# Optimization experiments

Hardware: AMD Instinct MI355X
Metric: run time of the kernel (lower is better)

## Reference

```python
import jax, jax.numpy as jnp
import numpy as np

B, L_IN, L_OUT, N, COV, EMB, H = 32, 336, 48, 512, 4, 32, 64
C = 1 + COV
D_IN = EMB + COV


def setup_inputs() -> dict:
    key = jax.random.key(0)
    ks = jax.random.split(key, 16)
    s = 1.0 / np.sqrt(H)

    def rn(k, shape, scale):
        return jax.random.normal(k, shape, jnp.float32) * scale

    return {
        "history_data": jax.random.normal(ks[0], (B, L_IN, N, C), jnp.float32),
        "future_data": jax.random.normal(ks[1], (B, L_OUT, N, C), jnp.float32),
        "emb_W": rn(ks[2], (EMB, 1), 0.5),
        "emb_b": rn(ks[3], (EMB,), 0.1),
        "W_ih0": rn(ks[4], (4 * H, D_IN), s),
        "W_hh0": rn(ks[5], (4 * H, H), s),
        "b_ih0": rn(ks[6], (4 * H,), s),
        "b_hh0": rn(ks[7], (4 * H,), s),
        "W_ih1": rn(ks[8], (4 * H, H), s),
        "W_hh1": rn(ks[9], (4 * H, H), s),
        "b_ih1": rn(ks[10], (4 * H,), s),
        "b_hh1": rn(ks[11], (4 * H,), s),
        "head_W": rn(ks[12], (2, H), s),
        "head_b": rn(ks[13], (2,), 0.1),
        "train": 1,
    }


def _lstm_cell(x_t, h, c, W_ih, W_hh, b_ih, b_hh):
    # gate order i, f, g, o (torch nn.LSTM convention)
    g = x_t @ W_ih.T + b_ih + h @ W_hh.T + b_hh
    i, f, gg, o = jnp.split(g, 4, axis=-1)
    c = jax.nn.sigmoid(f) * c + jax.nn.sigmoid(i) * jnp.tanh(gg)
    h = jax.nn.sigmoid(o) * jnp.tanh(c)
    return h, c


def _deepar_forward(history_data, future_data, emb_W, emb_b,
                    W_ih0, W_hh0, b_ih0, b_hh0,
                    W_ih1, W_hh1, b_ih1, b_hh1,
                    head_W, head_b):
    Bb, L_in, Nn, _ = history_data.shape
    L_out = future_data.shape[1]
    # [B, L_in+L_out, N, .]
    target = jnp.concatenate([history_data[..., 0:1], future_data[..., 0:1]], axis=1)
    covar = jnp.concatenate([history_data[..., 1:], future_data[..., 1:]], axis=1)
    # train=True branch: teacher forcing for t = 1 .. L-1
    prev = target[:, :-1]        # [B, T, N, 1]
    cov_t = covar[:, 1:]         # [B, T, N, COV]
    emb = prev @ emb_W.T + emb_b  # [B, T, N, EMB]
    x = jnp.concatenate([emb, cov_t], axis=-1)      # [B, T, N, EMB+COV]
    T = x.shape[1]
    x = x.transpose(1, 0, 2, 3).reshape(T, Bb * Nn, -1)  # scan over time
    Hh = W_hh0.shape[1]
    z = jnp.zeros((Bb * Nn, Hh), x.dtype)

    def step(carry, x_t):
        h0, c0, h1, c1 = carry
        h0, c0 = _lstm_cell(x_t, h0, c0, W_ih0, W_hh0, b_ih0, b_hh0)
        h1, c1 = _lstm_cell(h0, h1, c1, W_ih1, W_hh1, b_ih1, b_hh1)
        p = jax.nn.relu(h1) @ head_W.T + head_b       # [BN, 2]
        mu = p[:, 0:1]
        sigma = jax.nn.softplus(p[:, 1:2])
        return (h0, c0, h1, c1), jnp.concatenate([mu, sigma], axis=-1)

    _, outs = jax.lax.scan(step, (z, z, z, z), x)     # [T, BN, 2]
    outs = outs.reshape(T, Bb, Nn, 2).transpose(1, 0, 2, 3)  # [B, T, N, 2]
    return outs[:, -L_out:]


def reference(history_data, future_data, emb_W, emb_b,
              W_ih0, W_hh0, b_ih0, b_hh0,
              W_ih1, W_hh1, b_ih1, b_hh1,
              head_W, head_b, train):
    # train is a static Python int (1 = teacher forcing branch implemented here)
    return _deepar_forward(history_data, future_data, emb_W, emb_b,
                           W_ih0, W_hh0, b_ih0, b_hh0,
                           W_ih1, W_hh1, b_ih1, b_hh1,
                           head_W, head_b)
```

## Files before the change

kernel.cpp:

```cpp
#include <hip/hip_runtime.h>


#define T_STEPS 383
#define AST 168
#define LOG2E 1.44269504088896340736f

typedef __attribute__((ext_vector_type(8))) short short8;
typedef __attribute__((ext_vector_type(4))) float floatx4;

__device__ __forceinline__ unsigned short f2bf(float f){
  union { float f; unsigned u; } v; v.f = f;
  unsigned u = v.u + 0x7fffu + ((v.u >> 16) & 1u);
  return (unsigned short)(u >> 16);
}
__device__ __forceinline__ unsigned short f2bf_fast(float f){
  union { float f; unsigned u; } v; v.f = f;
  return (unsigned short)((v.u + 0x8000u) >> 16);
}
__device__ __forceinline__ float bf2f(unsigned short b){
  union { unsigned u; float f; } v; v.u = ((unsigned)b) << 16; return v.f;
}

__device__ __forceinline__ float lstm_h(float iv, float fv, float gv, float ov, float& c){
  const float ea = __builtin_amdgcn_exp2f(-fv);
  const float eb = __builtin_amdgcn_exp2f(-iv);
  const float ec = __builtin_amdgcn_exp2f(-gv);
  const float eo = __builtin_amdgcn_exp2f(-ov);
  const float A = 1.f + ea, B = 1.f + eb, C = 1.f + ec, D = 1.f + eo;
  const float BC = B * C;
  const float num = c * BC + A * (2.f - C);
  const float cn = num * __builtin_amdgcn_rcpf(A * BC);
  c = cn;
  const float arg = fminf(cn * (-2.f * LOG2E), 126.f);
  const float E = 1.f + __builtin_amdgcn_exp2f(arg);
  return (2.f - E) * __builtin_amdgcn_rcpf(D * E);
}

__global__ __launch_bounds__(256, 2) void deepar_kernel(
    const float* __restrict__ hist, const float* __restrict__ fut,
    const float* __restrict__ embW, const float* __restrict__ embB,
    const float* __restrict__ Wih0, const float* __restrict__ Whh0,
    const float* __restrict__ bih0, const float* __restrict__ bhh0,
    const float* __restrict__ Wih1, const float* __restrict__ Whh1,
    const float* __restrict__ bih1, const float* __restrict__ bhh1,
    const float* __restrict__ headW, const float* __restrict__ headB,
    float* __restrict__ outp)
{
  const int tid  = threadIdx.x;
  const int lane = tid & 63;
  const int wv   = tid >> 6;
  const int l15  = lane & 15;
  const int quad = lane >> 4;
  const int koff = quad * 8;
  const int jcol = wv * 16 + l15;

  const int b  = blockIdx.x >> 4;
  const int n0 = (blockIdx.x & 15) * 32;

  __shared__ __align__(16) unsigned short A[32 * AST];
  __shared__ __align__(16) unsigned short W1[256 * 128];
  __shared__ float HW[128];

  for (int i = tid; i < 32 * AST; i += 256) A[i] = 0;
  if (tid < 128) HW[tid] = headW[tid];
  const float hb0 = headB[0], hb1 = headB[1];

  short8 bf0[4][3];
  float  bi0[4], bi1[4];
  #pragma unroll
  for (int g = 0; g < 4; ++g){
    const float gsc = (g == 2) ? 2.f * LOG2E : LOG2E;
    const int r = g * 64 + wv * 16 + l15;
    float u = 0.f, bb = bih0[r] + bhh0[r];
    #pragma unroll
    for (int e = 0; e < 32; ++e){
      float wval = Wih0[r * 36 + e];
      u  += wval * embW[e];
      bb += wval * embB[e];
    }
    bi0[g] = bb * gsc;
    bi1[g] = (bih1[r] + bhh1[r]) * gsc;
    #pragma unroll
    for (int kf = 0; kf < 2; ++kf)
      #pragma unroll
      for (int j = 0; j < 8; ++j)
        bf0[g][kf][j] = (short)f2bf(Whh0[r * 64 + kf * 32 + koff + j] * gsc);
    #pragma unroll
    for (int j = 0; j < 8; ++j){
      int kk = koff + j;
      float v = 0.f;
      if (kk == 0) v = u;
      else if (kk >= 1 && kk <= 4) v = Wih0[r * 36 + 32 + (kk - 1)];
      bf0[g][2][j] = (short)f2bf(v * gsc);
    }
    #pragma unroll
    for (int kf = 0; kf < 4; ++kf){
      const float* src = (kf < 2) ? (Wih1 + r * 64 + kf * 32)
                                  : (Whh1 + r * 64 + (kf - 2) * 32);
      short8 w;
      #pragma unroll
      for (int j = 0; j < 8; ++j)
        w[j] = (short)f2bf(src[koff + j] * gsc);
      *(short8*)&W1[(((wv * 16 + g * 4 + kf) * 64) + lane) * 8] = w;
    }
  }

  const bool isPrev = (tid < 32);
  const bool isCov  = (tid >= 64 && tid < 192);
  int ss = 0, cc = 0;
  if (isPrev){ ss = tid; cc = 0; }
  if (isCov) { ss = (tid - 64) >> 2; cc = 1 + ((tid - 64) & 3); }
  const int myN = n0 + ss;

  auto loadSlab = [&](int tt) -> float {
    if (isPrev){
      int l = tt; if (l > 383) l = 383;
      return (l < 336) ? hist[(((size_t)b * 336 + l) * 512 + myN) * 5]
                       : fut [(((size_t)b * 48 + (l - 336)) * 512 + myN) * 5];
    } else if (isCov){
      int l = tt + 1; if (l > 383) l = 383;
      return (l < 336) ? hist[(((size_t)b * 336 + l) * 512 + myN) * 5 + cc]
                       : fut [(((size_t)b * 48 + (l - 336)) * 512 + myN) * 5 + cc];
    }
    return 0.f;
  };

  float rIn = loadSlab(0);
  if (isPrev || isCov) A[ss * AST + 128 + cc] = f2bf(rIn);
  rIn = loadSlab(1);

  float c0s[8], c1s[8];
  #pragma unroll
  for (int i = 0; i < 8; ++i){ c0s[i] = 0.f; c1s[i] = 0.f; }

  __syncthreads();

  for (int t = 0; t < T_STEPS; ++t){
    floatx4 acc[4][2];
    #pragma unroll
    for (int g = 0; g < 4; ++g)
      #pragma unroll
      for (int mt = 0; mt < 2; ++mt){
        floatx4 binit = { bi0[g], bi0[g], bi0[g], bi0[g] };
        acc[g][mt] = binit;
      }
    const int c0off[3] = { 0, 32, 128 };
    #pragma unroll
    for (int mt = 0; mt < 2; ++mt){
      #pragma unroll
      for (int kf = 0; kf < 3; ++kf){
        short8 af = *(const short8*)&A[(mt * 16 + l15) * AST + c0off[kf] + koff];
        #pragma unroll
        for (int g = 0; g < 4; ++g)
          acc[g][mt] = __builtin_amdgcn_mfma_f32_16x16x32_bf16(af, bf0[g][kf], acc[g][mt], 0, 0, 0);
      }
    }
    float hn[8];
    #pragma unroll
    for (int mt = 0; mt < 2; ++mt)
      #pragma unroll
      for (int q = 0; q < 4; ++q){
        int idx = mt * 4 + q;
        hn[idx] = lstm_h(acc[0][mt][q], acc[1][mt][q], acc[2][mt][q], acc[3][mt][q], c0s[idx]);
      }
    __syncthreads();
    #pragma unroll
    for (int mt = 0; mt < 2; ++mt)
      #pragma unroll
      for (int q = 0; q < 4; ++q){
        int s = mt * 16 + quad * 4 + q;
        A[s * AST + jcol] = f2bf_fast(hn[mt * 4 + q]);
      }
    if (isPrev || isCov) A[ss * AST + 128 + cc] = f2bf_fast(rIn);
    rIn = loadSlab(t + 2);
    __syncthreads();

    #pragma unroll
    for (int g = 0; g < 4; ++g)
      #pragma unroll
      for (int mt = 0; mt < 2; ++mt){
        floatx4 binit = { bi1[g], bi1[g], bi1[g], bi1[g] };
        acc[g][mt] = binit;
      }
    #pragma unroll
    for (int kf = 0; kf < 4; ++kf){
      short8 wfr[4];
      #pragma unroll
      for (int g = 0; g < 4; ++g)
        wfr[g] = *(const short8*)&W1[(((wv * 16 + g * 4 + kf) * 64) + lane) * 8];
      #pragma unroll
      for (int mt = 0; mt < 2; ++mt){
        short8 af = *(const short8*)&A[(mt * 16 + l15) * AST + kf * 32 + koff];
        #pragma unroll
        for (int g = 0; g < 4; ++g)
          acc[g][mt] = __builtin_amdgcn_mfma_f32_16x16x32_bf16(af, wfr[g], acc[g][mt], 0, 0, 0);
      }
    }
    #pragma unroll
    for (int mt = 0; mt < 2; ++mt)
      #pragma unroll
      for (int q = 0; q < 4; ++q){
        int idx = mt * 4 + q;
        hn[idx] = lstm_h(acc[0][mt][q], acc[1][mt][q], acc[2][mt][q], acc[3][mt][q], c1s[idx]);
      }
    __syncthreads();
    #pragma unroll
    for (int mt = 0; mt < 2; ++mt)
      #pragma unroll
      for (int q = 0; q < 4; ++q){
        int s = mt * 16 + quad * 4 + q;
        A[s * AST + 64 + jcol] = f2bf_fast(hn[mt * 4 + q]);
      }

    if (t >= 335){
      __syncthreads();
      const int hs = tid >> 3, outc = (tid >> 2) & 1, part = tid & 3;
      const short8 hv0 = *(const short8*)&A[hs * AST + 64 + part * 16];
      const short8 hv1 = *(const short8*)&A[hs * AST + 64 + part * 16 + 8];
      float p = 0.f;
      #pragma unroll
      for (int jj = 0; jj < 8; ++jj){
        float a0 = fmaxf(bf2f((unsigned short)hv0[jj]), 0.f);
        float a1 = fmaxf(bf2f((unsigned short)hv1[jj]), 0.f);
        p += a0 * HW[outc * 64 + part * 16 + jj];
        p += a1 * HW[outc * 64 + part * 16 + 8 + jj];
      }
      p += __shfl_xor(p, 1);
      p += __shfl_xor(p, 2);
      if ((tid & 3) == 0){
        float val;
        if (outc == 0) val = p + hb0;
        else {
          float x = p + hb1;
          val = fmaxf(x, 0.f) + __logf(1.f + __expf(-fabsf(x)));
        }
        outp[(((size_t)b * 48 + (t - 335)) * 512 + (n0 + hs)) * 2 + outc] = val;
      }
    }
  }
}

extern "C" void kernel_launch(void* const* d_in, const int* in_sizes, int n_in,
                              void* d_out, int out_size, void* d_ws, size_t ws_size,
                              hipStream_t stream) {
  (void)in_sizes; (void)n_in; (void)out_size; (void)d_ws; (void)ws_size;
  deepar_kernel<<<dim3(512), dim3(256), 0, stream>>>(
      (const float*)d_in[0],  (const float*)d_in[1],
      (const float*)d_in[2],  (const float*)d_in[3],
      (const float*)d_in[4],  (const float*)d_in[5],
      (const float*)d_in[6],  (const float*)d_in[7],
      (const float*)d_in[8],  (const float*)d_in[9],
      (const float*)d_in[10], (const float*)d_in[11],
      (const float*)d_in[12], (const float*)d_in[13],
      (float*)d_out);
}
```

Measured before the change: 1.268 ms.

## Double-buffer layer-1 hidden state in LDS to drop a per-step barrier

Layer-1 hidden state now ping-pongs between two LDS regions by step parity, and the row stride grows to hold the extra buffer. This removes the barrier before the layer-1 h write and the extra barrier before the output head. The head computation for the previous step is deferred into the next step's layer-0 phase, plus one final head call after the loop. It costs more LDS per block, which could limit occupancy or change bank conflict patterns.

```diff
diff --git a/kernel.cpp b/kernel.cpp
--- a/kernel.cpp
+++ b/kernel.cpp
@@ -2,7 +2,7 @@
 
 
 #define T_STEPS 383
-#define AST 168
+#define AST 232
 #define LOG2E 1.44269504088896340736f
 
 typedef __attribute__((ext_vector_type(8))) short short8;
@@ -133,9 +133,40 @@
   #pragma unroll
   for (int i = 0; i < 8; ++i){ c0s[i] = 0.f; c1s[i] = 0.f; }
 
+  const int hd_hs   = tid >> 3;
+  const int hd_outc = (tid >> 2) & 1;
+  const int hd_part = tid & 3;
+
+  auto headOp = [&](int tt, int reg){
+    const short8 hv0 = *(const short8*)&A[hd_hs * AST + reg + hd_part * 16];
+    const short8 hv1 = *(const short8*)&A[hd_hs * AST + reg + hd_part * 16 + 8];
+    float p = 0.f;
+    #pragma unroll
+    for (int jj = 0; jj < 8; ++jj){
+      float a0 = fmaxf(bf2f((unsigned short)hv0[jj]), 0.f);
+      float a1 = fmaxf(bf2f((unsigned short)hv1[jj]), 0.f);
+      p += a0 * HW[hd_outc * 64 + hd_part * 16 + jj];
+      p += a1 * HW[hd_outc * 64 + hd_part * 16 + 8 + jj];
+    }
+    p += __shfl_xor(p, 1);
+    p += __shfl_xor(p, 2);
+    if ((tid & 3) == 0){
+      float val;
+      if (hd_outc == 0) val = p + hb0;
+      else {
+        float x = p + hb1;
+        val = fmaxf(x, 0.f) + __logf(1.f + __expf(-fabsf(x)));
+      }
+      outp[(((size_t)b * 48 + (tt - 335)) * 512 + (n0 + hd_hs)) * 2 + hd_outc] = val;
+    }
+  };
+
   __syncthreads();
 
   for (int t = 0; t < T_STEPS; ++t){
+    const int h1rd = (t & 1) ? 64 : 144;
+    const int h1wr = (t & 1) ? 144 : 64;
+
     floatx4 acc[4][2];
     #pragma unroll
     for (int g = 0; g < 4; ++g)
@@ -173,6 +204,7 @@
       }
     if (isPrev || isCov) A[ss * AST + 128 + cc] = f2bf_fast(rIn);
     rIn = loadSlab(t + 2);
+    if (t >= 336) headOp(t - 1, h1rd);
     __syncthreads();
 
     #pragma unroll
@@ -182,6 +214,7 @@
         floatx4 binit = { bi1[g], bi1[g], bi1[g], bi1[g] };
         acc[g][mt] = binit;
       }
+    const int c1off[4] = { 0, 32, h1rd, h1rd + 32 };
     #pragma unroll
     for (int kf = 0; kf < 4; ++kf){
       short8 wfr[4];
@@ -190,7 +223,7 @@
         wfr[g] = *(const short8*)&W1[(((wv * 16 + g * 4 + kf) * 64) + lane) * 8];
       #pragma unroll
       for (int mt = 0; mt < 2; ++mt){
-        short8 af = *(const short8*)&A[(mt * 16 + l15) * AST + kf * 32 + koff];
+        short8 af = *(const short8*)&A[(mt * 16 + l15) * AST + c1off[kf] + koff];
         #pragma unroll
         for (int g = 0; g < 4; ++g)
           acc[g][mt] = __builtin_amdgcn_mfma_f32_16x16x32_bf16(af, wfr[g], acc[g][mt], 0, 0, 0);
@@ -203,41 +236,17 @@
         int idx = mt * 4 + q;
         hn[idx] = lstm_h(acc[0][mt][q], acc[1][mt][q], acc[2][mt][q], acc[3][mt][q], c1s[idx]);
       }
-    __syncthreads();
     #pragma unroll
     for (int mt = 0; mt < 2; ++mt)
       #pragma unroll
       for (int q = 0; q < 4; ++q){
         int s = mt * 16 + quad * 4 + q;
-        A[s * AST + 64 + jcol] = f2bf_fast(hn[mt * 4 + q]);
-      }
-
-    if (t >= 335){
-      __syncthreads();
-      const int hs = tid >> 3, outc = (tid >> 2) & 1, part = tid & 3;
-      const short8 hv0 = *(const short8*)&A[hs * AST + 64 + part * 16];
-      const short8 hv1 = *(const short8*)&A[hs * AST + 64 + part * 16 + 8];
-      float p = 0.f;
-      #pragma unroll
-      for (int jj = 0; jj < 8; ++jj){
-        float a0 = fmaxf(bf2f((unsigned short)hv0[jj]), 0.f);
-        float a1 = fmaxf(bf2f((unsigned short)hv1[jj]), 0.f);
-        p += a0 * HW[outc * 64 + part * 16 + jj];
-        p += a1 * HW[outc * 64 + part * 16 + 8 + jj];
-      }
-      p += __shfl_xor(p, 1);
-      p += __shfl_xor(p, 2);
-      if ((tid & 3) == 0){
-        float val;
-        if (outc == 0) val = p + hb0;
-        else {
-          float x = p + hb1;
-          val = fmaxf(x, 0.f) + __logf(1.f + __expf(-fabsf(x)));
-        }
-        outp[(((size_t)b * 48 + (t - 335)) * 512 + (n0 + hs)) * 2 + outc] = val;
-      }
-    }
+        A[s * AST + h1wr + jcol] = f2bf_fast(hn[mt * 4 + q]);
+      }
   }
+
+  __syncthreads();
+  headOp(382, 64);
 }
 
 extern "C" void kernel_launch(void* const* d_in, const int* in_sizes, int n_in,
```

After: 1.213 ms. 4.4% less time.
